# Kernel tuning notes

Hardware: AMD Instinct MI355X
Metric: run time of the kernel (lower is better)

The kernel has to match this reference:

```python
import jax, jax.numpy as jnp
import numpy as np


def setup_inputs() -> dict:
    key = jax.random.key(0)
    ks = jax.random.split(key, 6)
    B, V, T, Fin = 16, 12288, 4, 64
    Kv, Kt, Fout = 4, 4, 64
    NNZ = 9 * V  # ~8 neighbors + self loop per vertex (HEALPix)
    inputs = jax.random.normal(ks[0], (B, V, T, Fin), dtype=jnp.float32)
    std = np.sqrt(2.0 / (Fin * Kv * Kt))
    weight = jax.random.normal(ks[1], (Fin, Kv, Kt, Fout), dtype=jnp.float32) * std
    bias = jnp.zeros((Fout,), dtype=jnp.float32)
    lap_rows = jax.random.randint(ks[2], (NNZ,), 0, V, dtype=jnp.int32)
    lap_cols = jax.random.randint(ks[3], (NNZ,), 0, V, dtype=jnp.int32)
    # small values so the Chebyshev recurrence stays numerically tame
    lap_vals = jax.random.normal(ks[4], (NNZ,), dtype=jnp.float32) * 0.1
    return {"inputs": inputs, "weight": weight, "bias": bias,
            "lap_vals": lap_vals, "lap_rows": lap_rows, "lap_cols": lap_cols}


def _cheb_conv_temp(inputs, weight, lap_vals, lap_rows, lap_cols):
    B, V, T, Fin = inputs.shape
    Fin_w, Kv, Kt, Fout = weight.shape
    # x0: [V, T*Fin*B] matching torch permute(1,2,3,0).view
    x0 = jnp.transpose(inputs, (1, 2, 3, 0)).reshape(V, T * Fin * B)

    def spmm(x):  # sparse laplacian @ x via gather + segment_sum
        return jax.ops.segment_sum(lap_vals[:, None] * x[lap_cols], lap_rows,
                                   num_segments=V)

    xs = [x0]
    if Kv > 1:
        x1 = spmm(x0)
        xs.append(x1)
        for _ in range(2, Kv):
            x2 = 2.0 * spmm(x1) - x0
            xs.append(x2)
            x0, x1 = x1, x2
    x = jnp.stack(xs, axis=0).reshape(Kv, V, T, Fin, B)
    # contraction aligns flattened (Fin,Kv,T) of x with (Fin,Kv,Kt) of weight
    return jnp.einsum('kvtfb,fkto->bvo', x, weight)


def reference(inputs, weight, bias, lap_vals, lap_rows, lap_cols):
    out = _cheb_conv_temp(inputs, weight, lap_vals, lap_rows, lap_cols)
    return out + bias
```

## Files before the change

### kernel.cpp

```cpp
#include <hip/hip_runtime.h>

#define V_N 12288
#define B_N 16
#define TF_N 256
#define ROW2 1024
#define FOUT 64

typedef __attribute__((ext_vector_type(8))) short short8;
typedef __attribute__((ext_vector_type(4))) float f32x4;

__device__ __forceinline__ unsigned short f2bf(float x){
  unsigned u = __float_as_uint(x);
  return (unsigned short)((u + 0x7FFFu + ((u >> 16) & 1u)) >> 16);
}
__device__ __forceinline__ float bf2f(unsigned short h){
  return __uint_as_float(((unsigned)h) << 16);
}

__global__ void k_zero(int* __restrict__ p, int n){
  int i = blockIdx.x * 256 + threadIdx.x;
  if (i < n) p[i] = 0;
}

__global__ void k_hist(const int* __restrict__ rows, int* __restrict__ cnt, int nnz){
  int i = blockIdx.x * 256 + threadIdx.x;
  if (i < nnz) atomicAdd(&cnt[rows[i]], 1);
}

__global__ void k_scan(const int* __restrict__ cnt, int* __restrict__ rp){
  __shared__ int part[256];
  __shared__ int base[257];
  int t = threadIdx.x;
  const int per = V_N / 256;
  int s = 0;
  for (int i = 0; i < per; ++i) s += cnt[t * per + i];
  part[t] = s;
  __syncthreads();
  if (t == 0){
    int run = 0;
    for (int i = 0; i < 256; ++i){ base[i] = run; run += part[i]; }
    base[256] = run;
  }
  __syncthreads();
  int run = base[t];
  for (int i = 0; i < per; ++i){ rp[t * per + i] = run; run += cnt[t * per + i]; }
  if (t == 255) rp[V_N] = run;
}

__global__ void k_scatter(const int* __restrict__ rows, const int* __restrict__ cols,
                          const float* __restrict__ vals, const int* __restrict__ rp,
                          int* __restrict__ cur, int* __restrict__ cols_s,
                          float* __restrict__ vals_s, int nnz){
  int i = blockIdx.x * 256 + threadIdx.x;
  if (i < nnz){
    int r = rows[i];
    int pos = rp[r] + atomicAdd(&cur[r], 1);
    cols_s[pos] = cols[i];
    vals_s[pos] = vals[i];
  }
}

__global__ void k_convw(const float* __restrict__ w, unsigned short* __restrict__ wb){
  int i = blockIdx.x * 256 + threadIdx.x;
  int j = i & 7;
  int l = (i >> 3) & 63;
  int n = (i >> 9) & 3;
  int s = (i >> 11) & 7;
  int k = (i >> 14) & 3;
  int kk = s * 32 + ((l >> 4) << 3) + j;
  int t = kk >> 6, f = kk & 63;
  int o = (n << 4) + (l & 15);
  wb[i] = f2bf(w[((f * 4 + k) * 4 + t) * 64 + o]);
}

__global__ __launch_bounds__(256, 3) void k_proj(
                       const float* __restrict__ in, const unsigned short* __restrict__ wb,
                       unsigned short* __restrict__ y0, unsigned short* __restrict__ y1,
                       unsigned short* __restrict__ y2, unsigned short* __restrict__ y3){
  __shared__ unsigned short As[32 * 256];
  char* lds = (char*)As;
  int t = threadIdx.x;
  int vb = blockIdx.x >> 4;
  int b  = blockIdx.x & 15;
  int v0 = vb * 32;
  const float* src = in + ((size_t)b * V_N + v0) * TF_N;
  float4 f[8];
  #pragma unroll
  for (int i = 0; i < 8; ++i) f[i] = *(const float4*)(src + i * 1024 + t * 4);
  #pragma unroll
  for (int i = 0; i < 8; ++i){
    int flat = i * 1024 + t * 4;
    int r  = flat >> 8;
    int c2 = (flat & 255) * 2;
    unsigned long long pk =  (unsigned long long)f2bf(f[i].x)
                          | ((unsigned long long)f2bf(f[i].y) << 16)
                          | ((unsigned long long)f2bf(f[i].z) << 32)
                          | ((unsigned long long)f2bf(f[i].w) << 48);
    *(unsigned long long*)(lds + ((r * 512 + c2) ^ ((r & 7) << 4))) = pk;
  }
  __syncthreads();

  int lane = t & 63;
  int k    = t >> 6;
  int colL = lane & 15, rg = lane >> 4;
  f32x4 acc[2][4];
  #pragma unroll
  for (int mt = 0; mt < 2; ++mt)
    #pragma unroll
    for (int n = 0; n < 4; ++n) acc[mt][n] = (f32x4){0.f, 0.f, 0.f, 0.f};

  const unsigned short* wk = wb + k * 16384 + lane * 8;
  const char* aL0 = lds + (size_t)0;
  short8 wbuf[2][4];
  short8 abuf[2][2];
  #pragma unroll
  for (int n = 0; n < 4; ++n) wbuf[0][n] = *(const short8*)(wk + (n << 9));
  {
    int c2 = rg * 16;
    abuf[0][0] = *(const short8*)(lds + (( colL       * 512 + c2) ^ ((colL & 7) << 4)));
    abuf[0][1] = *(const short8*)(lds + (((16 + colL) * 512 + c2) ^ ((colL & 7) << 4)));
  }
  #pragma unroll
  for (int s = 0; s < 8; ++s){
    int cur = s & 1, nxt = cur ^ 1;
    if (s < 7){
      #pragma unroll
      for (int n = 0; n < 4; ++n)
        wbuf[nxt][n] = *(const short8*)(wk + (((s + 1) * 4 + n) << 9));
      int c2 = rg * 16 + (s + 1) * 64;
      abuf[nxt][0] = *(const short8*)(lds + (( colL       * 512 + c2) ^ ((colL & 7) << 4)));
      abuf[nxt][1] = *(const short8*)(lds + (((16 + colL) * 512 + c2) ^ ((colL & 7) << 4)));
    }
    #pragma unroll
    for (int n = 0; n < 4; ++n){
      acc[0][n] = __builtin_amdgcn_mfma_f32_16x16x32_bf16(abuf[cur][0], wbuf[cur][n], acc[0][n], 0, 0, 0);
      acc[1][n] = __builtin_amdgcn_mfma_f32_16x16x32_bf16(abuf[cur][1], wbuf[cur][n], acc[1][n], 0, 0, 0);
    }
  }
  unsigned short* yk = (k == 0) ? y0 : (k == 1) ? y1 : (k == 2) ? y2 : y3;
  #pragma unroll
  for (int mt = 0; mt < 2; ++mt)
    #pragma unroll
    for (int r = 0; r < 4; ++r){
      int v = v0 + mt * 16 + rg * 4 + r;
      unsigned lo = (unsigned)f2bf(acc[mt][0][r]) | ((unsigned)f2bf(acc[mt][1][r]) << 16);
      unsigned hi = (unsigned)f2bf(acc[mt][2][r]) | ((unsigned)f2bf(acc[mt][3][r]) << 16);
      uint2 pk = {lo, hi};
      *(uint2*)(yk + (size_t)v * ROW2 + b * 64 + colL * 4) = pk;
    }
}

__global__ void k_spmm2(const unsigned short* __restrict__ src,
                        const unsigned short* __restrict__ addA,
                        const unsigned short* __restrict__ subB,
                        unsigned short* __restrict__ dst,
                        const int* __restrict__ rp, const int* __restrict__ cols,
                        const float* __restrict__ vals, float alpha){
  int lane = threadIdx.x & 63;
  int r = blockIdx.x * 4 + (threadIdx.x >> 6);
  int j0 = lane * 16;
  float acc[16];
  #pragma unroll
  for (int p = 0; p < 16; ++p) acc[p] = 0.f;
  int beg = rp[r], end = rp[r + 1];
  for (int i = beg; i < end; ++i){
    float val = vals[i];
    int c = cols[i];
    const unsigned short* srow = src + (size_t)c * ROW2 + j0;
    short8 a0 = *(const short8*)srow;
    short8 a1 = *(const short8*)(srow + 8);
    #pragma unroll
    for (int p = 0; p < 8; ++p) acc[p]     += val * bf2f((unsigned short)a0[p]);
    #pragma unroll
    for (int p = 0; p < 8; ++p) acc[p + 8] += val * bf2f((unsigned short)a1[p]);
  }
  const unsigned short* arow = addA + (size_t)r * ROW2 + j0;
  short8 q0 = *(const short8*)arow;
  short8 q1 = *(const short8*)(arow + 8);
  #pragma unroll
  for (int p = 0; p < 8; ++p) acc[p]     = alpha * acc[p]     + bf2f((unsigned short)q0[p]);
  #pragma unroll
  for (int p = 0; p < 8; ++p) acc[p + 8] = alpha * acc[p + 8] + bf2f((unsigned short)q1[p]);
  if (subB){
    const unsigned short* brow = subB + (size_t)r * ROW2 + j0;
    short8 s0 = *(const short8*)brow;
    short8 s1 = *(const short8*)(brow + 8);
    #pragma unroll
    for (int p = 0; p < 8; ++p) acc[p]     -= bf2f((unsigned short)s0[p]);
    #pragma unroll
    for (int p = 0; p < 8; ++p) acc[p + 8] -= bf2f((unsigned short)s1[p]);
  }
  unsigned short* drow = dst + (size_t)r * ROW2 + j0;
  short8 o0, o1;
  #pragma unroll
  for (int p = 0; p < 8; ++p) o0[p] = (short)f2bf(acc[p]);
  #pragma unroll
  for (int p = 0; p < 8; ++p) o1[p] = (short)f2bf(acc[p + 8]);
  *(short8*)drow = o0;
  *(short8*)(drow + 8) = o1;
}

__global__ void k_final(const unsigned short* __restrict__ src,
                        const unsigned short* __restrict__ y0,
                        const unsigned short* __restrict__ b2,
                        const float* __restrict__ bias,
                        float* __restrict__ out,
                        const int* __restrict__ rp, const int* __restrict__ cols,
                        const float* __restrict__ vals){
  int lane = threadIdx.x & 63;
  int v = blockIdx.x * 4 + (threadIdx.x >> 6);
  int j0 = lane * 16;
  float acc[16];
  #pragma unroll
  for (int p = 0; p < 16; ++p) acc[p] = 0.f;
  int beg = rp[v], end = rp[v + 1];
  for (int i = beg; i < end; ++i){
    float val = vals[i];
    int c = cols[i];
    const unsigned short* srow = src + (size_t)c * ROW2 + j0;
    short8 a0 = *(const short8*)srow;
    short8 a1 = *(const short8*)(srow + 8);
    #pragma unroll
    for (int p = 0; p < 8; ++p) acc[p]     += val * bf2f((unsigned short)a0[p]);
    #pragma unroll
    for (int p = 0; p < 8; ++p) acc[p + 8] += val * bf2f((unsigned short)a1[p]);
  }
  const unsigned short* yrow = y0 + (size_t)v * ROW2 + j0;
  const unsigned short* brow = b2 + (size_t)v * ROW2 + j0;
  short8 q0 = *(const short8*)yrow;
  short8 q1 = *(const short8*)(yrow + 8);
  short8 s0 = *(const short8*)brow;
  short8 s1 = *(const short8*)(brow + 8);
  #pragma unroll
  for (int p = 0; p < 8; ++p) acc[p]     += bf2f((unsigned short)q0[p]) - bf2f((unsigned short)s0[p]);
  #pragma unroll
  for (int p = 0; p < 8; ++p) acc[p + 8] += bf2f((unsigned short)q1[p]) - bf2f((unsigned short)s1[p]);
  int b = lane >> 2;
  int c0 = (lane & 3) * 4;
  float* obase = out + ((size_t)b * V_N + v) * FOUT;
  #pragma unroll
  for (int n = 0; n < 4; ++n){
    float4 bv = *(const float4*)(bias + n * 16 + c0);
    float4 w;
    w.x = acc[0 * 4 + n] + bv.x;
    w.y = acc[1 * 4 + n] + bv.y;
    w.z = acc[2 * 4 + n] + bv.z;
    w.w = acc[3 * 4 + n] + bv.w;
    *(float4*)(obase + n * 16 + c0) = w;
  }
}

extern "C" void kernel_launch(void* const* d_in, const int* in_sizes, int n_in,
                              void* d_out, int out_size, void* d_ws, size_t ws_size,
                              hipStream_t stream) {
  const float* inputs   = (const float*)d_in[0];
  const float* weight   = (const float*)d_in[1];
  const float* bias     = (const float*)d_in[2];
  const float* lap_vals = (const float*)d_in[3];
  const int*   lap_rows = (const int*)d_in[4];
  const int*   lap_cols = (const int*)d_in[5];
  float* out = (float*)d_out;
  int nnz = in_sizes[3];

  char* ws = (char*)d_ws;
  size_t off = 0;
  auto alloc = [&](size_t bytes) -> void* {
    void* p = ws + off;
    off += (bytes + 255) & ~(size_t)255;
    return p;
  };
  const size_t YB = (size_t)V_N * ROW2 * 2;
  unsigned short* y0 = (unsigned short*)alloc(YB);
  unsigned short* y1 = (unsigned short*)alloc(YB);
  unsigned short* y2 = (unsigned short*)alloc(YB);
  unsigned short* y3 = (unsigned short*)alloc(YB);
  unsigned short* c2 = (unsigned short*)alloc(YB);
  unsigned short* c1 = (unsigned short*)alloc(YB);
  unsigned short* wb = (unsigned short*)alloc(65536 * 2);
  int*   cnt   = (int*)alloc(V_N * 4);
  int*   cur   = (int*)alloc(V_N * 4);
  int*   rp    = (int*)alloc((V_N + 1) * 4);
  int*   colss = (int*)alloc((size_t)nnz * 4);
  float* valss = (float*)alloc((size_t)nnz * 4);

  k_zero<<<(2 * V_N + 255) / 256, 256, 0, stream>>>(cnt, 2 * V_N);
  k_hist<<<(nnz + 255) / 256, 256, 0, stream>>>(lap_rows, cnt, nnz);
  k_scan<<<1, 256, 0, stream>>>(cnt, rp);
  k_scatter<<<(nnz + 255) / 256, 256, 0, stream>>>(lap_rows, lap_cols, lap_vals, rp, cur,
                                                   colss, valss, nnz);
  k_convw<<<65536 / 256, 256, 0, stream>>>(weight, wb);
  k_proj<<<(V_N / 32) * B_N, 256, 0, stream>>>(inputs, wb, y0, y1, y2, y3);

  k_spmm2<<<V_N / 4, 256, 0, stream>>>(y3, y2, nullptr, c2, rp, colss, valss, 2.0f);
  k_spmm2<<<V_N / 4, 256, 0, stream>>>(c2, y1, y3, c1, rp, colss, valss, 2.0f);
  k_final<<<V_N / 4, 256, 0, stream>>>(c1, y0, c2, bias, out, rp, colss, valss);
}
```

Baseline: 234.9 us.

## Make projection kernel persistent over tiles with register-resident weights and prefetch

Each block of the projection GEMM now processes eight (vertex-block, batch) tiles instead of one. The full weight slice stays in registers across tiles, and the next tile's input is prefetched into registers while the current tile is computed, using a double-buffered LDS area. The aim is to remove repeated weight loads per tile and to overlap global input loads with MFMA work. In exchange it launches fewer blocks (768), lowers the occupancy hint to 2, and raises register pressure from holding 32 short8 weight vectors.

```diff
diff --git a/kernel.cpp b/kernel.cpp
--- a/kernel.cpp
+++ b/kernel.cpp
@@ -5,6 +5,7 @@
 #define TF_N 256
 #define ROW2 1024
 #define FOUT 64
+#define TPB_TILES 8
 
 typedef __attribute__((ext_vector_type(8))) short short8;
 typedef __attribute__((ext_vector_type(4))) float f32x4;
@@ -73,81 +74,92 @@
   wb[i] = f2bf(w[((f * 4 + k) * 4 + t) * 64 + o]);
 }
 
-__global__ __launch_bounds__(256, 3) void k_proj(
+__global__ __launch_bounds__(256, 2) void k_proj(
                        const float* __restrict__ in, const unsigned short* __restrict__ wb,
                        unsigned short* __restrict__ y0, unsigned short* __restrict__ y1,
                        unsigned short* __restrict__ y2, unsigned short* __restrict__ y3){
-  __shared__ unsigned short As[32 * 256];
-  char* lds = (char*)As;
+  __shared__ unsigned short As[2][32 * 256];
   int t = threadIdx.x;
-  int vb = blockIdx.x >> 4;
-  int b  = blockIdx.x & 15;
-  int v0 = vb * 32;
-  const float* src = in + ((size_t)b * V_N + v0) * TF_N;
-  float4 f[8];
-  #pragma unroll
-  for (int i = 0; i < 8; ++i) f[i] = *(const float4*)(src + i * 1024 + t * 4);
-  #pragma unroll
-  for (int i = 0; i < 8; ++i){
-    int flat = i * 1024 + t * 4;
-    int r  = flat >> 8;
-    int c2 = (flat & 255) * 2;
-    unsigned long long pk =  (unsigned long long)f2bf(f[i].x)
-                          | ((unsigned long long)f2bf(f[i].y) << 16)
-                          | ((unsigned long long)f2bf(f[i].z) << 32)
-                          | ((unsigned long long)f2bf(f[i].w) << 48);
-    *(unsigned long long*)(lds + ((r * 512 + c2) ^ ((r & 7) << 4))) = pk;
-  }
-  __syncthreads();
-
   int lane = t & 63;
   int k    = t >> 6;
   int colL = lane & 15, rg = lane >> 4;
-  f32x4 acc[2][4];
-  #pragma unroll
-  for (int mt = 0; mt < 2; ++mt)
-    #pragma unroll
-    for (int n = 0; n < 4; ++n) acc[mt][n] = (f32x4){0.f, 0.f, 0.f, 0.f};
-
-  const unsigned short* wk = wb + k * 16384 + lane * 8;
-  const char* aL0 = lds + (size_t)0;
-  short8 wbuf[2][4];
-  short8 abuf[2][2];
-  #pragma unroll
-  for (int n = 0; n < 4; ++n) wbuf[0][n] = *(const short8*)(wk + (n << 9));
+
+  int tile0 = blockIdx.x * TPB_TILES;
+
+  float4 r[8];
   {
-    int c2 = rg * 16;
-    abuf[0][0] = *(const short8*)(lds + (( colL       * 512 + c2) ^ ((colL & 7) << 4)));
-    abuf[0][1] = *(const short8*)(lds + (((16 + colL) * 512 + c2) ^ ((colL & 7) << 4)));
-  }
-  #pragma unroll
-  for (int s = 0; s < 8; ++s){
-    int cur = s & 1, nxt = cur ^ 1;
-    if (s < 7){
+    int vb = tile0 >> 4, b = tile0 & 15;
+    const float* src = in + ((size_t)b * V_N + vb * 32) * TF_N;
+    #pragma unroll
+    for (int i = 0; i < 8; ++i) r[i] = *(const float4*)(src + i * 1024 + t * 4);
+  }
+
+  short8 W[8][4];
+  {
+    const unsigned short* wk = wb + k * 16384 + lane * 8;
+    #pragma unroll
+    for (int s = 0; s < 8; ++s)
       #pragma unroll
       for (int n = 0; n < 4; ++n)
-        wbuf[nxt][n] = *(const short8*)(wk + (((s + 1) * 4 + n) << 9));
-      int c2 = rg * 16 + (s + 1) * 64;
-      abuf[nxt][0] = *(const short8*)(lds + (( colL       * 512 + c2) ^ ((colL & 7) << 4)));
-      abuf[nxt][1] = *(const short8*)(lds + (((16 + colL) * 512 + c2) ^ ((colL & 7) << 4)));
+        W[s][n] = *(const short8*)(wk + (((s * 4 + n)) << 9));
+  }
+  unsigned short* yk = (k == 0) ? y0 : (k == 1) ? y1 : (k == 2) ? y2 : y3;
+
+  for (int ti = 0; ti < TPB_TILES; ++ti){
+    int ft = tile0 + ti;
+    char* lds = (char*)As[ti & 1];
+    #pragma unroll
+    for (int i = 0; i < 8; ++i){
+      int flat = i * 1024 + t * 4;
+      int row = flat >> 8;
+      int c2  = (flat & 255) * 2;
+      unsigned long long pk =  (unsigned long long)f2bf(r[i].x)
+                            | ((unsigned long long)f2bf(r[i].y) << 16)
+                            | ((unsigned long long)f2bf(r[i].z) << 32)
+                            | ((unsigned long long)f2bf(r[i].w) << 48);
+      *(unsigned long long*)(lds + ((row * 512 + c2) ^ ((row & 7) << 4))) = pk;
     }
-    #pragma unroll
-    for (int n = 0; n < 4; ++n){
-      acc[0][n] = __builtin_amdgcn_mfma_f32_16x16x32_bf16(abuf[cur][0], wbuf[cur][n], acc[0][n], 0, 0, 0);
-      acc[1][n] = __builtin_amdgcn_mfma_f32_16x16x32_bf16(abuf[cur][1], wbuf[cur][n], acc[1][n], 0, 0, 0);
+    if (ti + 1 < TPB_TILES){
+      int ft1 = ft + 1;
+      int vb = ft1 >> 4, b = ft1 & 15;
+      const float* src = in + ((size_t)b * V_N + vb * 32) * TF_N;
+      #pragma unroll
+      for (int i = 0; i < 8; ++i) r[i] = *(const float4*)(src + i * 1024 + t * 4);
     }
-  }
-  unsigned short* yk = (k == 0) ? y0 : (k == 1) ? y1 : (k == 2) ? y2 : y3;
-  #pragma unroll
-  for (int mt = 0; mt < 2; ++mt)
-    #pragma unroll
-    for (int r = 0; r < 4; ++r){
-      int v = v0 + mt * 16 + rg * 4 + r;
-      unsigned lo = (unsigned)f2bf(acc[mt][0][r]) | ((unsigned)f2bf(acc[mt][1][r]) << 16);
-      unsigned hi = (unsigned)f2bf(acc[mt][2][r]) | ((unsigned)f2bf(acc[mt][3][r]) << 16);
-      uint2 pk = {lo, hi};
-      *(uint2*)(yk + (size_t)v * ROW2 + b * 64 + colL * 4) = pk;
+    __syncthreads();
+
+    f32x4 acc[2][4];
+    #pragma unroll
+    for (int mt = 0; mt < 2; ++mt)
+      #pragma unroll
+      for (int n = 0; n < 4; ++n) acc[mt][n] = (f32x4){0.f, 0.f, 0.f, 0.f};
+
+    #pragma unroll
+    for (int s = 0; s < 8; ++s){
+      int c2 = rg * 16 + s * 64;
+      short8 a0 = *(const short8*)(lds + (( colL       * 512 + c2) ^ ((colL & 7) << 4)));
+      short8 a1 = *(const short8*)(lds + (((16 + colL) * 512 + c2) ^ ((colL & 7) << 4)));
+      #pragma unroll
+      for (int n = 0; n < 4; ++n){
+        acc[0][n] = __builtin_amdgcn_mfma_f32_16x16x32_bf16(a0, W[s][n], acc[0][n], 0, 0, 0);
+        acc[1][n] = __builtin_amdgcn_mfma_f32_16x16x32_bf16(a1, W[s][n], acc[1][n], 0, 0, 0);
+      }
     }
+    {
+      int vb = ft >> 4, b = ft & 15, v0 = vb * 32;
+      #pragma unroll
+      for (int mt = 0; mt < 2; ++mt)
+        #pragma unroll
+        for (int q = 0; q < 4; ++q){
+          int v = v0 + mt * 16 + rg * 4 + q;
+          unsigned lo = (unsigned)f2bf(acc[mt][0][q]) | ((unsigned)f2bf(acc[mt][1][q]) << 16);
+          unsigned hi = (unsigned)f2bf(acc[mt][2][q]) | ((unsigned)f2bf(acc[mt][3][q]) << 16);
+          uint2 pk = {lo, hi};
+          *(uint2*)(yk + (size_t)v * ROW2 + b * 64 + colL * 4) = pk;
+        }
+    }
+    __syncthreads();
+  }
 }
 
 __global__ void k_spmm2(const unsigned short* __restrict__ src,
@@ -289,7 +301,7 @@
   k_scatter<<<(nnz + 255) / 256, 256, 0, stream>>>(lap_rows, lap_cols, lap_vals, rp, cur,
                                                    colss, valss, nnz);
   k_convw<<<65536 / 256, 256, 0, stream>>>(weight, wb);
-  k_proj<<<(V_N / 32) * B_N, 256, 0, stream>>>(inputs, wb, y0, y1, y2, y3);
+  k_proj<<<(V_N / 32) * B_N / TPB_TILES, 256, 0, stream>>>(inputs, wb, y0, y1, y2, y3);
 
   k_spmm2<<<V_N / 4, 256, 0, stream>>>(y3, y2, nullptr, c2, rp, colss, valss, 2.0f);
   k_spmm2<<<V_N / 4, 256, 0, stream>>>(c2, y1, y3, c1, rp, colss, valss, 2.0f);
```

New measurement: 216.1 us. 1.09x faster.
